# Kernel optimization log

Measured on AMD Instinct MI355X. Metric: run time of the kernel, lower is better.

Reference implementation:

```python
import jax, jax.numpy as jnp
import numpy as np

N, D, H, E, TOP_K = 4096, 2048, 8192, 8, 2
CAPACITY_FACTOR = 1.25
WORLD_SIZE = 1  # single-process reference (dist.all_reduce is identity)


def setup_inputs() -> dict:
    key = jax.random.key(0)
    ks = jax.random.split(key, 7)
    s = 0.02
    return {
        "x": jax.random.normal(ks[0], (N, D), dtype=jnp.float32),
        "router_w": jax.random.normal(ks[1], (D, E), dtype=jnp.float32) * s,
        "router_b": jnp.zeros((E,), dtype=jnp.float32),
        "w1": jax.random.normal(ks[2], (E, D, H), dtype=jnp.float32) * s,
        "b1": jnp.zeros((E, H), dtype=jnp.float32),
        "w2": jax.random.normal(ks[3], (E, H, D), dtype=jnp.float32) * s,
        "b2": jnp.zeros((E, D), dtype=jnp.float32),
    }


def _moe_forward(x, router_w, router_b, w1, b1, w2, b2):
    n, d = x.shape
    e = w1.shape[0]
    capacity = max(int(CAPACITY_FACTOR * n / (TOP_K * WORLD_SIZE)), 1)

    # Router
    logits = x @ router_w + router_b                       # [N, E]
    probs = jax.nn.softmax(logits, axis=-1)
    expert_weights, expert_indices = jax.lax.top_k(probs, TOP_K)  # [N, K]

    eids = jnp.arange(e)
    # Per-(expert, token) selection mask and routing weight
    hit = expert_indices[None, :, :] == eids[:, None, None]       # [E, N, K]
    sel = hit.any(-1)                                             # [E, N]
    w_tok = jnp.sum(jnp.where(hit, expert_weights[None], 0.0), axis=-1)  # [E, N]

    # Capacity truncation: keep first `capacity` selected tokens (in order)
    rank = jnp.cumsum(sel, axis=1) - 1                            # [E, N]
    keep = sel & (rank < capacity)
    pos = jnp.where(keep, jnp.arange(n)[None, :], n)
    idx = jnp.sort(pos, axis=1)[:, :capacity]                     # [E, C]
    valid = idx < n
    idx_c = jnp.where(valid, idx, 0)

    # Gather -> grouped expert MLP -> weighted scatter-add combine
    xg = x[idx_c]                                                 # [E, C, D]
    h = jax.nn.gelu(jnp.einsum('ecd,edh->ech', xg, w1) + b1[:, None, :], approximate=False)
    y = jnp.einsum('ech,ehd->ecd', h, w2) + b2[:, None, :]        # [E, C, D]
    wg = jnp.take_along_axis(w_tok, idx_c, axis=1) * valid        # [E, C]
    contrib = y * wg[:, :, None]
    final = jnp.zeros_like(x).at[idx_c.reshape(-1)].add(contrib.reshape(-1, d))

    # Auxiliary losses (world_size = 1)
    expert_count = sel.sum(axis=1).astype(probs.dtype)            # [E]
    usage = expert_count / (n * WORLD_SIZE)
    density = probs.mean(axis=0)
    balance_loss = jnp.sum(density * usage) * e
    important = probs.sum(axis=0)
    important_loss = jnp.mean(important ** 2)
    aux_loss = balance_loss + important_loss
    return final, aux_loss


def reference(x, router_w, router_b, w1, b1, w2, b2):
    return _moe_forward(x, router_w, router_b, w1, b1, w2, b2)
```

## Files before the change

### kernel.cpp

```cpp
#include <hip/hip_runtime.h>
#include <hip/hip_bf16.h>
#include <math.h>

#define N_TOK 4096
#define DIM   2048
#define HID   8192
#define NE    8
#define CAP   2560

#define BM 128
#define BN 128
#define BK 64

typedef __attribute__((ext_vector_type(4))) float f32x4;
typedef __attribute__((ext_vector_type(8))) short s16x8;

__device__ __forceinline__ unsigned short f2bf(float f) {
  unsigned int u = __builtin_bit_cast(unsigned int, f);
  u += 0x7fffu + ((u >> 16) & 1u);
  return (unsigned short)(u >> 16);
}

__device__ __forceinline__ void async16(const void* g, void* l) {
  __builtin_amdgcn_global_load_lds(
      (const __attribute__((address_space(1))) unsigned int*)g,
      (__attribute__((address_space(3))) unsigned int*)l, 16, 0, 0);
}

__device__ __forceinline__ float gelu_f(float v) {
  float z = v * 0.70710678118f;
  float az = fabsf(z);
  float t = __builtin_amdgcn_rcpf(1.0f + 0.3275911f * az);
  float p = ((((1.061405429f * t - 1.453152027f) * t + 1.421413741f) * t
              - 0.284496736f) * t + 0.254829592f) * t;
  float ex = __expf(-z * z);
  float erfa = 1.0f - p * ex;
  float erfz = copysignf(erfa, z);
  return 0.5f * v * (1.0f + erfz);
}

__global__ __launch_bounds__(256) void k_transpose64(const float* __restrict__ in,
                                                     unsigned short* __restrict__ out,
                                                     int R, int C, long inStr, long outStr) {
  __shared__ unsigned short tile[64][66];
  const float* ip = in + (long)blockIdx.z * inStr;
  unsigned short* op = out + (long)blockIdx.z * outStr;
  int c0 = blockIdx.x * 64, r0 = blockIdx.y * 64;
  int t = threadIdx.x;
  {
    int lr = t >> 4, lc = (t & 15) * 4;
#pragma unroll
    for (int p = 0; p < 4; ++p) {
      int row = lr + p * 16;
      float4 v = *(const float4*)(ip + (long)(r0 + row) * C + c0 + lc);
      ushort2 o0; o0.x = f2bf(v.x); o0.y = f2bf(v.y);
      ushort2 o1; o1.x = f2bf(v.z); o1.y = f2bf(v.w);
      *(ushort2*)&tile[row][lc] = o0;
      *(ushort2*)&tile[row][lc + 2] = o1;
    }
  }
  __syncthreads();
  {
    int orr = (t & 15) * 4, oc = t >> 4;
#pragma unroll
    for (int q = 0; q < 4; ++q) {
      int col = oc + q * 16;
      ushort4 o;
      o.x = tile[orr][col]; o.y = tile[orr + 1][col];
      o.z = tile[orr + 2][col]; o.w = tile[orr + 3][col];
      *(ushort4*)(op + (long)(c0 + col) * R + r0 + orr) = o;
    }
  }
}

__global__ __launch_bounds__(256) void k_router(const float* __restrict__ x,
                                                const float* __restrict__ rw,
                                                const float* __restrict__ rb,
                                                int* __restrict__ eidx,
                                                float* __restrict__ ew,
                                                float* __restrict__ imp) {
  __shared__ float simp[NE];
  int tid = threadIdx.x, lane = tid & 63, wv = tid >> 6;
  if (tid < NE) simp[tid] = 0.f;
  __syncthreads();
  int t = blockIdx.x * 4 + wv;
  float acc[NE] = {};
  const float* xr = x + (long)t * DIM;
  for (int i = 0; i < DIM / 64; ++i) {
    int k = i * 64 + lane;
    float xv = xr[k];
    const float4* wr4 = (const float4*)(rw + (long)k * NE);
    float4 w0 = wr4[0], w1v = wr4[1];
    acc[0] += xv * w0.x;  acc[1] += xv * w0.y;  acc[2] += xv * w0.z;  acc[3] += xv * w0.w;
    acc[4] += xv * w1v.x; acc[5] += xv * w1v.y; acc[6] += xv * w1v.z; acc[7] += xv * w1v.w;
  }
#pragma unroll
  for (int e = 0; e < NE; e++) {
#pragma unroll
    for (int off = 32; off >= 1; off >>= 1) acc[e] += __shfl_down(acc[e], off);
  }
  if (lane == 0) {
    float l[NE], p[NE];
    float mx = -1e30f;
#pragma unroll
    for (int e = 0; e < NE; e++) { l[e] = acc[e] + rb[e]; mx = fmaxf(mx, l[e]); }
    float s = 0.f;
#pragma unroll
    for (int e = 0; e < NE; e++) { p[e] = expf(l[e] - mx); s += p[e]; }
    float inv = 1.f / s;
#pragma unroll
    for (int e = 0; e < NE; e++) p[e] *= inv;
    int a0 = 0;
#pragma unroll
    for (int e = 1; e < NE; e++) if (p[e] > p[a0]) a0 = e;
    int a1 = (a0 == 0) ? 1 : 0;
#pragma unroll
    for (int e = 0; e < NE; e++) if (e != a0 && p[e] > p[a1]) a1 = e;
    eidx[t * 2] = a0; eidx[t * 2 + 1] = a1;
    ew[t * 2] = p[a0]; ew[t * 2 + 1] = p[a1];
#pragma unroll
    for (int e = 0; e < NE; e++) atomicAdd(&simp[e], p[e]);
  }
  __syncthreads();
  if (tid < NE) atomicAdd(&imp[tid], simp[tid]);
}

__global__ void k_build(const int* __restrict__ eidx, const float* __restrict__ ew,
                        int* __restrict__ idxc, float* __restrict__ wg,
                        int* __restrict__ cnt_raw, int* __restrict__ cnt_cap) {
  int e = blockIdx.x;
  int lane = threadIdx.x;
  int base = 0;
  for (int t0 = 0; t0 < N_TOK; t0 += 64) {
    int t = t0 + lane;
    int e0 = eidx[t * 2], e1 = eidx[t * 2 + 1];
    bool sel = (e0 == e) || (e1 == e);
    unsigned long long m = __ballot(sel);
    if (sel) {
      int r = base + __popcll(m & ((1ull << lane) - 1ull));
      if (r < CAP) {
        idxc[e * CAP + r] = t;
        wg[e * CAP + r] = (e0 == e) ? ew[t * 2] : ew[t * 2 + 1];
      }
    }
    base += __popcll(m);
  }
  if (lane == 0) { cnt_raw[e] = base; cnt_cap[e] = base < CAP ? base : CAP; }
}

__global__ __launch_bounds__(256) void k_gatherf(const float* __restrict__ x,
                                                 const int* __restrict__ idxc,
                                                 const int* __restrict__ cnt_cap,
                                                 unsigned short* __restrict__ xg) {
  int row = blockIdx.x;
  if ((row % CAP) >= cnt_cap[row / CAP]) return;
  int tok = idxc[row];
  const float* s = x + (long)tok * DIM;
  unsigned short* d = xg + (long)row * DIM;
  int c = threadIdx.x * 8;
  float4 a = *(const float4*)(s + c);
  float4 b = *(const float4*)(s + c + 4);
  ushort4 o0; o0.x = f2bf(a.x); o0.y = f2bf(a.y); o0.z = f2bf(a.z); o0.w = f2bf(a.w);
  ushort4 o1; o1.x = f2bf(b.x); o1.y = f2bf(b.y); o1.z = f2bf(b.z); o1.w = f2bf(b.w);
  *(ushort4*)(d + c) = o0;
  *(ushort4*)(d + c + 4) = o1;
}

template <int EPI>
__global__ __launch_bounds__(256, 3) void k_gemm(
    const unsigned short* __restrict__ Abase, long Astr,
    const unsigned short* __restrict__ Bbase, long Bstr,
    const float* __restrict__ biasBase, int biasStr,
    void* outBase, long outStr,
    const int* __restrict__ cnt_cap,
    const int* __restrict__ idxc, const float* __restrict__ wgv,
    int K, int Nout, int e_base) {
  int nwg = gridDim.x * gridDim.y * gridDim.z;
  int bid = blockIdx.x + gridDim.x * (blockIdx.y + gridDim.y * blockIdx.z);
  int chunk = nwg >> 3;
  int nbid = (bid & 7) * chunk + (bid >> 3);
  int bx = nbid % gridDim.x;
  int rest = nbid / gridDim.x;
  int by = rest % gridDim.y;
  int bz = rest / gridDim.y;

  int e = e_base + bz;
  int cnt = cnt_cap[e];
  int m0 = bx * BM;
  if (m0 >= cnt) return;
  int n0 = by * BN;
  const unsigned short* A = Abase + (long)e * Astr;
  const unsigned short* B = Bbase + (long)e * Bstr;
  __shared__ unsigned short Als[BM * BK];
  __shared__ unsigned short Bls[BN * BK];
  int tid = threadIdx.x, lane = tid & 63;
  int wv = tid >> 6, wr = wv >> 1, wc = wv & 1;
  f32x4 acc[4][4] = {};

  for (int kt = 0; kt < K; kt += BK) {
#pragma unroll
    for (int s = 0; s < 4; s++) {
      int c = s * 256 + tid;
      int row = c >> 3, k16 = c & 7;
      int sk = k16 ^ (row & 7);
      async16(A + (long)(m0 + row) * K + kt + sk * 8, (char*)Als + c * 16);
    }
#pragma unroll
    for (int s = 0; s < 4; s++) {
      int c = s * 256 + tid;
      int row = c >> 3, k16 = c & 7;
      int sk = k16 ^ (row & 7);
      async16(B + (long)(n0 + row) * K + kt + sk * 8, (char*)Bls + c * 16);
    }
    __syncthreads();
#pragma unroll
    for (int kk = 0; kk < 2; kk++) {
      s16x8 af[4], bfr[4];
#pragma unroll
      for (int t4 = 0; t4 < 4; t4++) {
        int ar = wr * 64 + t4 * 16 + (lane & 15);
        int br = wc * 64 + t4 * 16 + (lane & 15);
        int kb = kk * 64 + (lane >> 4) * 16;
        af[t4]  = *(const s16x8*)((const char*)Als + ar * 128 + (kb ^ ((ar & 7) << 4)));
        bfr[t4] = *(const s16x8*)((const char*)Bls + br * 128 + (kb ^ ((br & 7) << 4)));
      }
#pragma unroll
      for (int i = 0; i < 4; i++)
#pragma unroll
        for (int j = 0; j < 4; j++)
          acc[i][j] = __builtin_amdgcn_mfma_f32_16x16x32_bf16(af[i], bfr[j], acc[i][j], 0, 0, 0);
    }
    __syncthreads();
  }

  const float* bias = biasBase + (long)e * biasStr;
  if constexpr (EPI == 1) {
    unsigned short* hout = (unsigned short*)outBase + (long)e * outStr;
#pragma unroll
    for (int j = 0; j < 4; j++) {
      int col = n0 + wc * 64 + j * 16 + (lane & 15);
      float bv = bias[col];
#pragma unroll
      for (int i = 0; i < 4; i++) {
        int rb0 = m0 + wr * 64 + i * 16 + (lane >> 4) * 4;
#pragma unroll
        for (int r = 0; r < 4; r++) {
          float v = acc[i][j][r] + bv;
          hout[(long)(rb0 + r) * Nout + col] = f2bf(gelu_f(v));
        }
      }
    }
  } else {
    float* fin = (float*)outBase;
#pragma unroll
    for (int i = 0; i < 4; i++) {
      int rb0 = m0 + wr * 64 + i * 16 + (lane >> 4) * 4;
      float4 w4 = *(const float4*)(wgv + e * CAP + rb0);
      int4 t4v = *(const int4*)(idxc + e * CAP + rb0);
      float wa[4] = {w4.x, w4.y, w4.z, w4.w};
      int ta[4] = {t4v.x, t4v.y, t4v.z, t4v.w};
#pragma unroll
      for (int r = 0; r < 4; r++) {
        float w = wa[r];
        if (w != 0.f) {
          int tok = ta[r];
#pragma unroll
          for (int j = 0; j < 4; j++) {
            int col = n0 + wc * 64 + j * 16 + (lane & 15);
            float v = (acc[i][j][r] + bias[col]) * w;
            atomicAdd(fin + (long)tok * Nout + col, v);
          }
        }
      }
    }
  }
}

__global__ void k_aux(const float* __restrict__ imp, const int* __restrict__ cnt,
                      float* __restrict__ out) {
  if (threadIdx.x == 0) {
    float bal = 0.f, il = 0.f;
    for (int e = 0; e < NE; e++) {
      bal += (imp[e] / (float)N_TOK) * ((float)cnt[e] / (float)N_TOK);
      il += imp[e] * imp[e];
    }
    out[0] = bal * (float)NE + il / (float)NE;
  }
}

extern "C" void kernel_launch(void* const* d_in, const int* in_sizes, int n_in,
                              void* d_out, int out_size, void* d_ws, size_t ws_size,
                              hipStream_t stream) {
  const float* x  = (const float*)d_in[0];
  const float* rw = (const float*)d_in[1];
  const float* rb = (const float*)d_in[2];
  const float* w1 = (const float*)d_in[3];
  const float* b1 = (const float*)d_in[4];
  const float* w2 = (const float*)d_in[5];
  const float* b2 = (const float*)d_in[6];
  float* out = (float*)d_out;

  char* ws = (char*)d_ws;
  size_t off = 0;
  auto alloc = [&](size_t bytes) -> char* {
    char* p = ws + off;
    off = (off + bytes + 255) & ~(size_t)255;
    return p;
  };
  float* imp     = (float*)alloc(NE * 4);
  int*   cnt_raw = (int*)alloc(NE * 4);
  int*   cnt_cap = (int*)alloc(NE * 4);
  int*   idxc    = (int*)alloc((size_t)NE * CAP * 4);
  float* wg      = (float*)alloc((size_t)NE * CAP * 4);
  int*   eidx    = (int*)alloc((size_t)N_TOK * 2 * 4);
  float* ew      = (float*)alloc((size_t)N_TOK * 2 * 4);
  size_t ctrl_end = off;
  unsigned short* xg = (unsigned short*)alloc((size_t)NE * CAP * DIM * 2);

  size_t need_grouped = off + (size_t)NE * DIM * HID * 2 * 2
                            + (size_t)NE * CAP * HID * 2 + 4096;
  bool grouped = ws_size >= need_grouped;

  unsigned short *w1t, *w2t, *hbuf;
  if (grouped) {
    w1t  = (unsigned short*)alloc((size_t)NE * DIM * HID * 2);
    w2t  = (unsigned short*)alloc((size_t)NE * HID * DIM * 2);
    hbuf = (unsigned short*)alloc((size_t)NE * CAP * HID * 2);
  } else {
    w1t  = (unsigned short*)alloc((size_t)DIM * HID * 2);
    w2t  = (unsigned short*)alloc((size_t)HID * DIM * 2);
    hbuf = (unsigned short*)alloc((size_t)CAP * HID * 2);
  }

  hipMemsetAsync(d_out, 0, ((size_t)N_TOK * DIM + 1) * 4, stream);
  hipMemsetAsync(d_ws, 0, ctrl_end, stream);

  k_router<<<N_TOK / 4, 256, 0, stream>>>(x, rw, rb, eidx, ew, imp);
  k_build<<<NE, 64, 0, stream>>>(eidx, ew, idxc, wg, cnt_raw, cnt_cap);
  k_gatherf<<<NE * CAP, 256, 0, stream>>>(x, idxc, cnt_cap, xg);

  if (grouped) {
    k_transpose64<<<dim3(HID / 64, DIM / 64, NE), 256, 0, stream>>>(
        w1, w1t, DIM, HID, (long)DIM * HID, (long)DIM * HID);
    k_transpose64<<<dim3(DIM / 64, HID / 64, NE), 256, 0, stream>>>(
        w2, w2t, HID, DIM, (long)HID * DIM, (long)HID * DIM);
    k_gemm<1><<<dim3(CAP / BM, HID / BN, NE), 256, 0, stream>>>(
        xg, (long)CAP * DIM, w1t, (long)HID * DIM, b1, HID,
        hbuf, (long)CAP * HID, cnt_cap, nullptr, nullptr, DIM, HID, 0);
    k_gemm<2><<<dim3(CAP / BM, DIM / BN, NE), 256, 0, stream>>>(
        hbuf, (long)CAP * HID, w2t, (long)DIM * HID, b2, DIM,
        d_out, 0, cnt_cap, idxc, wg, HID, DIM, 0);
  } else {
    for (int e = 0; e < NE; e++) {
      k_transpose64<<<dim3(HID / 64, DIM / 64, 1), 256, 0, stream>>>(
          w1 + (long)e * DIM * HID, w1t, DIM, HID, 0, 0);
      k_gemm<1><<<dim3(CAP / BM, HID / BN, 1), 256, 0, stream>>>(
          xg, (long)CAP * DIM, w1t, 0, b1, HID,
          hbuf, 0, cnt_cap, nullptr, nullptr, DIM, HID, e);
      k_transpose64<<<dim3(DIM / 64, HID / 64, 1), 256, 0, stream>>>(
          w2 + (long)e * HID * DIM, w2t, HID, DIM, 0, 0);
      k_gemm<2><<<dim3(CAP / BM, DIM / BN, 1), 256, 0, stream>>>(
          hbuf, 0, w2t, 0, b2, DIM,
          d_out, 0, cnt_cap, idxc, wg, HID, DIM, e);
    }
  }
  k_aux<<<1, 64, 0, stream>>>(imp, cnt_raw, out + (size_t)N_TOK * DIM);
}
```

Baseline: 1.172 ms.

## Fuse weight fp32-to-bf16 transpose into GEMM B-tile loads

Removes the separate transpose kernels that converted w1/w2 into bf16 K-major copies. The GEMM now reads fp32 weights directly with float4 loads, converts them to bf16 in registers, and writes the transposed, swizzled tile into LDS. This drops a full read-write pass over 512MB of fp32 weights and the transposed buffers from the workspace. In exchange, every M-tile re-reads fp32 weights, doubling B bytes and repeating the conversion. The B loads are also now synchronous register loads instead of async global-to-LDS copies.

```diff
diff --git a/kernel.cpp b/kernel.cpp
--- a/kernel.cpp
+++ b/kernel.cpp
@@ -37,40 +37,6 @@
   float erfa = 1.0f - p * ex;
   float erfz = copysignf(erfa, z);
   return 0.5f * v * (1.0f + erfz);
-}
-
-__global__ __launch_bounds__(256) void k_transpose64(const float* __restrict__ in,
-                                                     unsigned short* __restrict__ out,
-                                                     int R, int C, long inStr, long outStr) {
-  __shared__ unsigned short tile[64][66];
-  const float* ip = in + (long)blockIdx.z * inStr;
-  unsigned short* op = out + (long)blockIdx.z * outStr;
-  int c0 = blockIdx.x * 64, r0 = blockIdx.y * 64;
-  int t = threadIdx.x;
-  {
-    int lr = t >> 4, lc = (t & 15) * 4;
-#pragma unroll
-    for (int p = 0; p < 4; ++p) {
-      int row = lr + p * 16;
-      float4 v = *(const float4*)(ip + (long)(r0 + row) * C + c0 + lc);
-      ushort2 o0; o0.x = f2bf(v.x); o0.y = f2bf(v.y);
-      ushort2 o1; o1.x = f2bf(v.z); o1.y = f2bf(v.w);
-      *(ushort2*)&tile[row][lc] = o0;
-      *(ushort2*)&tile[row][lc + 2] = o1;
-    }
-  }
-  __syncthreads();
-  {
-    int orr = (t & 15) * 4, oc = t >> 4;
-#pragma unroll
-    for (int q = 0; q < 4; ++q) {
-      int col = oc + q * 16;
-      ushort4 o;
-      o.x = tile[orr][col]; o.y = tile[orr + 1][col];
-      o.z = tile[orr + 2][col]; o.w = tile[orr + 3][col];
-      *(ushort4*)(op + (long)(c0 + col) * R + r0 + orr) = o;
-    }
-  }
 }
 
 __global__ __launch_bounds__(256) void k_router(const float* __restrict__ x,
@@ -169,7 +135,7 @@
 template <int EPI>
 __global__ __launch_bounds__(256, 3) void k_gemm(
     const unsigned short* __restrict__ Abase, long Astr,
-    const unsigned short* __restrict__ Bbase, long Bstr,
+    const float* __restrict__ Bbase, long Bstr,
     const float* __restrict__ biasBase, int biasStr,
     void* outBase, long outStr,
     const int* __restrict__ cnt_cap,
@@ -190,7 +156,7 @@
   if (m0 >= cnt) return;
   int n0 = by * BN;
   const unsigned short* A = Abase + (long)e * Astr;
-  const unsigned short* B = Bbase + (long)e * Bstr;
+  const float* Bp = Bbase + (long)e * Bstr;
   __shared__ unsigned short Als[BM * BK];
   __shared__ unsigned short Bls[BN * BK];
   int tid = threadIdx.x, lane = tid & 63;
@@ -206,11 +172,25 @@
       async16(A + (long)(m0 + row) * K + kt + sk * 8, (char*)Als + c * 16);
     }
 #pragma unroll
-    for (int s = 0; s < 4; s++) {
-      int c = s * 256 + tid;
-      int row = c >> 3, k16 = c & 7;
-      int sk = k16 ^ (row & 7);
-      async16(B + (long)(n0 + row) * K + kt + sk * 8, (char*)Bls + c * 16);
+    for (int h = 0; h < 2; h++) {
+      int b = tid + h * 256;
+      int bn = (b & 31) * 4;
+      int bk = (b >> 5) * 4;
+      float4 r0 = *(const float4*)(Bp + (long)(kt + bk + 0) * Nout + n0 + bn);
+      float4 r1 = *(const float4*)(Bp + (long)(kt + bk + 1) * Nout + n0 + bn);
+      float4 r2 = *(const float4*)(Bp + (long)(kt + bk + 2) * Nout + n0 + bn);
+      float4 r3 = *(const float4*)(Bp + (long)(kt + bk + 3) * Nout + n0 + bn);
+      const float* rr[4] = {(const float*)&r0, (const float*)&r1,
+                            (const float*)&r2, (const float*)&r3};
+#pragma unroll
+      for (int i = 0; i < 4; i++) {
+        ushort4 o;
+        o.x = f2bf(rr[0][i]); o.y = f2bf(rr[1][i]);
+        o.z = f2bf(rr[2][i]); o.w = f2bf(rr[3][i]);
+        int row = bn + i;
+        int kbyte = bk * 2;
+        *(ushort4*)((char*)Bls + row * 128 + (kbyte ^ ((row & 7) << 4))) = o;
+      }
     }
     __syncthreads();
 #pragma unroll
@@ -317,20 +297,12 @@
   size_t ctrl_end = off;
   unsigned short* xg = (unsigned short*)alloc((size_t)NE * CAP * DIM * 2);
 
-  size_t need_grouped = off + (size_t)NE * DIM * HID * 2 * 2
-                            + (size_t)NE * CAP * HID * 2 + 4096;
+  size_t need_grouped = off + (size_t)NE * CAP * HID * 2 + 4096;
   bool grouped = ws_size >= need_grouped;
 
-  unsigned short *w1t, *w2t, *hbuf;
-  if (grouped) {
-    w1t  = (unsigned short*)alloc((size_t)NE * DIM * HID * 2);
-    w2t  = (unsigned short*)alloc((size_t)NE * HID * DIM * 2);
-    hbuf = (unsigned short*)alloc((size_t)NE * CAP * HID * 2);
-  } else {
-    w1t  = (unsigned short*)alloc((size_t)DIM * HID * 2);
-    w2t  = (unsigned short*)alloc((size_t)HID * DIM * 2);
-    hbuf = (unsigned short*)alloc((size_t)CAP * HID * 2);
-  }
+  unsigned short* hbuf;
+  if (grouped) hbuf = (unsigned short*)alloc((size_t)NE * CAP * HID * 2);
+  else         hbuf = (unsigned short*)alloc((size_t)CAP * HID * 2);
 
   hipMemsetAsync(d_out, 0, ((size_t)N_TOK * DIM + 1) * 4, stream);
   hipMemsetAsync(d_ws, 0, ctrl_end, stream);
@@ -340,27 +312,19 @@
   k_gatherf<<<NE * CAP, 256, 0, stream>>>(x, idxc, cnt_cap, xg);
 
   if (grouped) {
-    k_transpose64<<<dim3(HID / 64, DIM / 64, NE), 256, 0, stream>>>(
-        w1, w1t, DIM, HID, (long)DIM * HID, (long)DIM * HID);
-    k_transpose64<<<dim3(DIM / 64, HID / 64, NE), 256, 0, stream>>>(
-        w2, w2t, HID, DIM, (long)HID * DIM, (long)HID * DIM);
     k_gemm<1><<<dim3(CAP / BM, HID / BN, NE), 256, 0, stream>>>(
-        xg, (long)CAP * DIM, w1t, (long)HID * DIM, b1, HID,
+        xg, (long)CAP * DIM, w1, (long)DIM * HID, b1, HID,
         hbuf, (long)CAP * HID, cnt_cap, nullptr, nullptr, DIM, HID, 0);
     k_gemm<2><<<dim3(CAP / BM, DIM / BN, NE), 256, 0, stream>>>(
-        hbuf, (long)CAP * HID, w2t, (long)DIM * HID, b2, DIM,
+        hbuf, (long)CAP * HID, w2, (long)HID * DIM, b2, DIM,
         d_out, 0, cnt_cap, idxc, wg, HID, DIM, 0);
   } else {
     for (int e = 0; e < NE; e++) {
-      k_transpose64<<<dim3(HID / 64, DIM / 64, 1), 256, 0, stream>>>(
-          w1 + (long)e * DIM * HID, w1t, DIM, HID, 0, 0);
       k_gemm<1><<<dim3(CAP / BM, HID / BN, 1), 256, 0, stream>>>(
-          xg, (long)CAP * DIM, w1t, 0, b1, HID,
+          xg, (long)CAP * DIM, w1 + (long)e * DIM * HID, 0, b1, HID,
           hbuf, 0, cnt_cap, nullptr, nullptr, DIM, HID, e);
-      k_transpose64<<<dim3(DIM / 64, HID / 64, 1), 256, 0, stream>>>(
-          w2 + (long)e * HID * DIM, w2t, HID, DIM, 0, 0);
       k_gemm<2><<<dim3(CAP / BM, DIM / BN, 1), 256, 0, stream>>>(
-          hbuf, 0, w2t, 0, b2, DIM,
+          hbuf, 0, w2 + (long)e * HID * DIM, 0, b2, DIM,
           d_out, 0, cnt_cap, idxc, wg, HID, DIM, e);
     }
   }
```

Measured after the change: 1.455 ms. +24.1%, slower.
